# Kernel optimization log

Hardware: AMD Instinct MI355X
Metric: run time of the kernel (lower is better)

Reference implementation:

```python
import jax, jax.numpy as jnp
import numpy as np


def _bilinear_sample(plane, coords):
    """Bilinear grid_sample, align_corners=True, padding_mode='border'.
    plane: [C, S, S]; coords: [N, 2] with (x=width, y=height) in [-1, 1].
    Returns [N, C]."""
    C, S, _ = plane.shape
    scale = 0.5 * (S - 1)
    # align_corners=True mapping: -1 -> 0, +1 -> S-1; border padding == clamp
    px = jnp.clip((coords[:, 0] + 1.0) * scale, 0.0, S - 1.0)
    py = jnp.clip((coords[:, 1] + 1.0) * scale, 0.0, S - 1.0)
    x0 = jnp.floor(px).astype(jnp.int32)
    y0 = jnp.floor(py).astype(jnp.int32)
    x1 = jnp.minimum(x0 + 1, S - 1)
    y1 = jnp.minimum(y0 + 1, S - 1)
    wx = px - x0.astype(px.dtype)
    wy = py - y0.astype(py.dtype)
    v00 = plane[:, y0, x0]  # [C, N]
    v01 = plane[:, y0, x1]
    v10 = plane[:, y1, x0]
    v11 = plane[:, y1, x1]
    top = v00 * (1.0 - wx) + v01 * wx
    bot = v10 * (1.0 - wx) + v11 * wx
    return (top * (1.0 - wy) + bot * wy).T  # [N, C]


def setup_inputs() -> dict:
    key = jax.random.key(0)
    k1, k2 = jax.random.split(key)
    N, INDIM = 1000000, 4
    FDIM, FSIZE = 16, 1024
    P = INDIM * (INDIM - 1) // 2  # 6 plane pairs
    x = jax.random.uniform(k1, (N, INDIM), dtype=jnp.float32, minval=-1.0, maxval=1.0)
    fm = jax.random.normal(k2, (P, FDIM, FSIZE + 1, FSIZE + 1), dtype=jnp.float32) * 0.01
    return {"x": x, "fm": fm}


def reference(x, fm):
    N, indim = x.shape
    pairs = [(i, j) for i in range(indim - 1) for j in range(i + 1, indim)]
    ii = jnp.array([p[0] for p in pairs])
    jj = jnp.array([p[1] for p in pairs])
    # coords per plane pair: grid_sample convention (x=dim i, y=dim j)
    coords = jnp.stack([x[:, ii], x[:, jj]], axis=-1)      # [N, P, 2]
    coords = jnp.transpose(coords, (1, 0, 2))              # [P, N, 2]
    samples = jax.vmap(_bilinear_sample)(fm, coords)       # [P, N, fdim]
    # torch code concatenates pair features along dim 1 in pair order
    return jnp.transpose(samples, (1, 0, 2)).reshape(N, -1)  # [N, P*fdim]
```

## Files before the change

### kernel.cpp

```cpp
#include <hip/hip_runtime.h>
#include <stdint.h>


#define FP_S 1025
#define FP_C 16
#define FP_P 6

typedef float f32x4 __attribute__((ext_vector_type(4)));

__global__ __launch_bounds__(256) void fp_rowquant_v(const float* __restrict__ fm,
                                                     uint4* __restrict__ q8,
                                                     float* __restrict__ rs) {
    const size_t plane = (size_t)FP_S * FP_S;
    int y = blockIdx.x;
    int p = blockIdx.z;
    int t = threadIdx.x;
    const float* rowbase = fm + (size_t)p * FP_C * plane + (size_t)y * FP_S;

    f32x4 v[FP_C];
    float m = 0.0f;
#pragma unroll
    for (int c = 0; c < FP_C; ++c) {
        v[c] = *(const f32x4*)(rowbase + (size_t)c * plane + 4 * t);
        m = fmaxf(m, fmaxf(fmaxf(fabsf(v[c][0]), fabsf(v[c][1])),
                           fmaxf(fabsf(v[c][2]), fabsf(v[c][3]))));
    }
    float tail[FP_C];
    if (t == 255) {
#pragma unroll
        for (int c = 0; c < FP_C; ++c) {
            tail[c] = rowbase[(size_t)c * plane + 1024];
            m = fmaxf(m, fabsf(tail[c]));
        }
    }

    __shared__ float red[256];
    red[t] = m;
    __syncthreads();
#pragma unroll
    for (int s = 128; s > 0; s >>= 1) {
        if (t < s) red[t] = fmaxf(red[t], red[t + s]);
        __syncthreads();
    }
    float am = red[0];
    float inv = (am > 0.0f) ? 127.0f / am : 0.0f;
    if (t == 0) rs[p * FP_S + y] = am * (1.0f / 127.0f);

    uint4* qrow = q8 + (size_t)p * plane + (size_t)y * FP_S;
#pragma unroll
    for (int k = 0; k < 4; ++k) {
        uint32_t w[4];
#pragma unroll
        for (int r = 0; r < 4; ++r) {
            uint32_t acc = 0;
#pragma unroll
            for (int b = 0; b < 4; ++b) {
                int q = (int)rintf(v[4 * r + b][k] * inv);
                q = q > 127 ? 127 : (q < -127 ? -127 : q);
                acc |= ((uint32_t)(q & 0xff)) << (8 * b);
            }
            w[r] = acc;
        }
        qrow[4 * t + k] = make_uint4(w[0], w[1], w[2], w[3]);
    }
    if (t == 255) {
        uint32_t w[4];
#pragma unroll
        for (int r = 0; r < 4; ++r) {
            uint32_t acc = 0;
#pragma unroll
            for (int b = 0; b < 4; ++b) {
                int q = (int)rintf(tail[4 * r + b] * inv);
                q = q > 127 ? 127 : (q < -127 ? -127 : q);
                acc |= ((uint32_t)(q & 0xff)) << (8 * b);
            }
            w[r] = acc;
        }
        qrow[1024] = make_uint4(w[0], w[1], w[2], w[3]);
    }
}

__device__ __forceinline__ float fp_b8(uint32_t w, int b) {
    return (float)((int)(w << (24 - 8 * b)) >> 24);
}

__device__ __forceinline__ void fp_pair(int p, int& ii, int& jj) {
    switch (p) {
        case 0: ii = 0; jj = 1; break;
        case 1: ii = 0; jj = 2; break;
        case 2: ii = 0; jj = 3; break;
        case 3: ii = 1; jj = 2; break;
        case 4: ii = 1; jj = 3; break;
        default: ii = 2; jj = 3; break;
    }
}

__global__ __launch_bounds__(256) void fp_sample_q8r(const float* __restrict__ xin,
                                                     const uint4* __restrict__ q8,
                                                     const float* __restrict__ rs,
                                                     float* __restrict__ out, int N) {
    int n = blockIdx.x * 256 + threadIdx.x;
    if (n >= N) return;
    int p = blockIdx.z;
    int ii, jj;
    fp_pair(p, ii, jj);

    float4 xr = ((const float4*)xin)[n];
    float xv = (ii == 0) ? xr.x : ((ii == 1) ? xr.y : xr.z);
    float yv = (jj == 1) ? xr.y : ((jj == 2) ? xr.z : xr.w);

    float px = fminf(fmaxf((xv + 1.0f) * 512.0f, 0.0f), 1024.0f);
    float py = fminf(fmaxf((yv + 1.0f) * 512.0f, 0.0f), 1024.0f);
    float fx0 = floorf(px), fy0 = floorf(py);
    int x0 = (int)fx0, y0 = (int)fy0;
    int x1 = min(x0 + 1, FP_S - 1);
    int y1 = min(y0 + 1, FP_S - 1);
    float wx = px - fx0, wy = py - fy0;

    const float* prs = rs + p * FP_S;
    float s0 = prs[y0], s1 = prs[y1];
    float w00 = (1.0f - wx) * (1.0f - wy) * s0;
    float w01 = wx * (1.0f - wy) * s0;
    float w10 = (1.0f - wx) * wy * s1;
    float w11 = wx * wy * s1;

    const int plane = FP_S * FP_S;
    const uint4* pq = q8 + (size_t)p * plane;
    uint4 qa = pq[y0 * FP_S + x0];
    uint4 qb = pq[y0 * FP_S + x1];
    uint4 qc = pq[y1 * FP_S + x0];
    uint4 qd = pq[y1 * FP_S + x1];

    uint32_t wa[4] = {qa.x, qa.y, qa.z, qa.w};
    uint32_t wb[4] = {qb.x, qb.y, qb.z, qb.w};
    uint32_t wc[4] = {qc.x, qc.y, qc.z, qc.w};
    uint32_t wd[4] = {qd.x, qd.y, qd.z, qd.w};

    f32x4* o = (f32x4*)(out + (size_t)n * (FP_P * FP_C) + p * FP_C);
#pragma unroll
    for (int r = 0; r < 4; ++r) {
        f32x4 rr;
#pragma unroll
        for (int bb = 0; bb < 4; ++bb) {
            rr[bb] = w00 * fp_b8(wa[r], bb) + w01 * fp_b8(wb[r], bb) +
                     w10 * fp_b8(wc[r], bb) + w11 * fp_b8(wd[r], bb);
        }
        o[r] = rr;
    }
}

__global__ __launch_bounds__(256) void fp_sample_direct(const float* __restrict__ xin,
                                                        const float* __restrict__ fm,
                                                        float* __restrict__ out, int N) {
    int n = blockIdx.x * 256 + threadIdx.x;
    if (n >= N) return;
    int p = blockIdx.z;
    int ii, jj;
    fp_pair(p, ii, jj);

    float4 xr = ((const float4*)xin)[n];
    float xv = (ii == 0) ? xr.x : ((ii == 1) ? xr.y : xr.z);
    float yv = (jj == 1) ? xr.y : ((jj == 2) ? xr.z : xr.w);

    float px = fminf(fmaxf((xv + 1.0f) * 512.0f, 0.0f), 1024.0f);
    float py = fminf(fmaxf((yv + 1.0f) * 512.0f, 0.0f), 1024.0f);
    float fx0 = floorf(px), fy0 = floorf(py);
    int x0 = (int)fx0, y0 = (int)fy0;
    int x1 = min(x0 + 1, FP_S - 1);
    int y1 = min(y0 + 1, FP_S - 1);
    float wx = px - fx0, wy = py - fy0;
    float w00 = (1.0f - wx) * (1.0f - wy), w01 = wx * (1.0f - wy);
    float w10 = (1.0f - wx) * wy, w11 = wx * wy;

    const size_t plane = (size_t)FP_S * FP_S;
    const float* pl = fm + (size_t)p * FP_C * plane;
    float res[FP_C];
#pragma unroll
    for (int c = 0; c < FP_C; ++c) {
        const float* plc = pl + (size_t)c * plane;
        float a = plc[(size_t)y0 * FP_S + x0];
        float bq = plc[(size_t)y0 * FP_S + x1];
        float g = plc[(size_t)y1 * FP_S + x0];
        float d = plc[(size_t)y1 * FP_S + x1];
        res[c] = a * w00 + bq * w01 + g * w10 + d * w11;
    }
    f32x4* o = (f32x4*)(out + (size_t)n * (FP_P * FP_C) + p * FP_C);
#pragma unroll
    for (int k = 0; k < 4; ++k) {
        f32x4 r = {res[4 * k], res[4 * k + 1], res[4 * k + 2], res[4 * k + 3]};
        o[k] = r;
    }
}

static inline size_t fp_align(size_t v) { return (v + 255) & ~(size_t)255; }

extern "C" void kernel_launch(void* const* d_in, const int* in_sizes, int n_in,
                              void* d_out, int out_size, void* d_ws, size_t ws_size,
                              hipStream_t stream) {
    const float* x = (const float*)d_in[0];
    const float* fm = (const float*)d_in[1];
    float* out = (float*)d_out;
    int N = in_sizes[0] / 4;

    const size_t plane = (size_t)FP_S * FP_S;
    size_t q8_bytes = (size_t)FP_P * plane * 16;
    size_t rs_off = fp_align(q8_bytes);
    size_t needed = rs_off + (size_t)FP_P * FP_S * sizeof(float);

    if (ws_size >= needed) {
        uint4* q8 = (uint4*)d_ws;
        float* rs = (float*)((char*)d_ws + rs_off);

        dim3 gQ(FP_S, 1, FP_P);
        fp_rowquant_v<<<gQ, 256, 0, stream>>>(fm, q8, rs);

        dim3 gS((unsigned)((N + 255) / 256), 1, FP_P);
        fp_sample_q8r<<<gS, 256, 0, stream>>>(x, q8, rs, out, N);
    } else {
        dim3 gS((unsigned)((N + 255) / 256), 1, FP_P);
        fp_sample_direct<<<gS, 256, 0, stream>>>(x, fm, out, N);
    }
}
```

Measured before the change: 436.6 us.

## Quantize feature planes in 2x2 quad-tiled int8 layout with per-row-pair scales

Switches the int8 quantized plane from row-major texel order to a 2x2 quad-blocked layout, so the four bilinear neighbors of a sample usually fall in one contiguous 64-byte block. The per-row scale becomes a scale shared by each pair of rows, and the quantization kernel now handles two rows per 512-thread block. This aims to cut scattered cache-line traffic in the sampling kernel. In exchange, scales are coarser, which adds quantization error, and the padded last quad column adds a little workspace.

```diff
diff --git a/kernel.cpp b/kernel.cpp
--- a/kernel.cpp
+++ b/kernel.cpp
@@ -5,78 +5,100 @@
 #define FP_S 1025
 #define FP_C 16
 #define FP_P 6
-
+#define FP_Q 513
+
+typedef float f32x2 __attribute__((ext_vector_type(2)));
 typedef float f32x4 __attribute__((ext_vector_type(4)));
 
-__global__ __launch_bounds__(256) void fp_rowquant_v(const float* __restrict__ fm,
-                                                     uint4* __restrict__ q8,
-                                                     float* __restrict__ rs) {
+__device__ __forceinline__ int fp_qsat(float v, float inv) {
+    int q = (int)rintf(v * inv);
+    return q > 127 ? 127 : (q < -127 ? -127 : q);
+}
+
+__device__ __forceinline__ uint32_t fp_q4(float a, float b, float c, float d, float inv) {
+    return ((uint32_t)(fp_qsat(a, inv) & 0xff)) | ((uint32_t)(fp_qsat(b, inv) & 0xff) << 8) |
+           ((uint32_t)(fp_qsat(c, inv) & 0xff) << 16) | ((uint32_t)(fp_qsat(d, inv) & 0xff) << 24);
+}
+
+__device__ __forceinline__ uint4 fp_pack16v(const f32x2* v, int comp, float inv) {
+    uint4 r;
+    r.x = fp_q4(v[0][comp], v[1][comp], v[2][comp], v[3][comp], inv);
+    r.y = fp_q4(v[4][comp], v[5][comp], v[6][comp], v[7][comp], inv);
+    r.z = fp_q4(v[8][comp], v[9][comp], v[10][comp], v[11][comp], inv);
+    r.w = fp_q4(v[12][comp], v[13][comp], v[14][comp], v[15][comp], inv);
+    return r;
+}
+
+__device__ __forceinline__ uint4 fp_pack16s(const float* v, float inv) {
+    uint4 r;
+    r.x = fp_q4(v[0], v[1], v[2], v[3], inv);
+    r.y = fp_q4(v[4], v[5], v[6], v[7], inv);
+    r.z = fp_q4(v[8], v[9], v[10], v[11], inv);
+    r.w = fp_q4(v[12], v[13], v[14], v[15], inv);
+    return r;
+}
+
+__global__ __launch_bounds__(512) void fp_quadquant(const float* __restrict__ fm,
+                                                    uint4* __restrict__ q8,
+                                                    float* __restrict__ rs) {
     const size_t plane = (size_t)FP_S * FP_S;
-    int y = blockIdx.x;
+    int Y = blockIdx.x;
     int p = blockIdx.z;
     int t = threadIdx.x;
-    const float* rowbase = fm + (size_t)p * FP_C * plane + (size_t)y * FP_S;
-
-    f32x4 v[FP_C];
+    int y0 = 2 * Y;
+    bool hasy1 = (y0 + 1) < FP_S;
+    const float* pb = fm + (size_t)p * FP_C * plane;
+    const float* r0 = pb + (size_t)y0 * FP_S;
+    const float* r1 = hasy1 ? r0 + FP_S : r0;
+
+    f32x2 v0[FP_C], v1[FP_C];
     float m = 0.0f;
+    int x = 2 * t;
 #pragma unroll
     for (int c = 0; c < FP_C; ++c) {
-        v[c] = *(const f32x4*)(rowbase + (size_t)c * plane + 4 * t);
-        m = fmaxf(m, fmaxf(fmaxf(fabsf(v[c][0]), fabsf(v[c][1])),
-                           fmaxf(fabsf(v[c][2]), fabsf(v[c][3]))));
-    }
-    float tail[FP_C];
-    if (t == 255) {
+        v0[c] = *(const f32x2*)(r0 + (size_t)c * plane + x);
+        v1[c] = *(const f32x2*)(r1 + (size_t)c * plane + x);
+        m = fmaxf(m, fmaxf(fmaxf(fabsf(v0[c][0]), fabsf(v0[c][1])),
+                           fmaxf(fabsf(v1[c][0]), fabsf(v1[c][1]))));
+    }
+    if (t == 0) {
 #pragma unroll
         for (int c = 0; c < FP_C; ++c) {
-            tail[c] = rowbase[(size_t)c * plane + 1024];
-            m = fmaxf(m, fabsf(tail[c]));
+            m = fmaxf(m, fabsf(r0[(size_t)c * plane + 1024]));
+            m = fmaxf(m, fabsf(r1[(size_t)c * plane + 1024]));
         }
     }
 
-    __shared__ float red[256];
+    __shared__ float red[512];
     red[t] = m;
     __syncthreads();
 #pragma unroll
-    for (int s = 128; s > 0; s >>= 1) {
+    for (int s = 256; s > 0; s >>= 1) {
         if (t < s) red[t] = fmaxf(red[t], red[t + s]);
         __syncthreads();
     }
     float am = red[0];
     float inv = (am > 0.0f) ? 127.0f / am : 0.0f;
-    if (t == 0) rs[p * FP_S + y] = am * (1.0f / 127.0f);
-
-    uint4* qrow = q8 + (size_t)p * plane + (size_t)y * FP_S;
-#pragma unroll
-    for (int k = 0; k < 4; ++k) {
-        uint32_t w[4];
-#pragma unroll
-        for (int r = 0; r < 4; ++r) {
-            uint32_t acc = 0;
-#pragma unroll
-            for (int b = 0; b < 4; ++b) {
-                int q = (int)rintf(v[4 * r + b][k] * inv);
-                q = q > 127 ? 127 : (q < -127 ? -127 : q);
-                acc |= ((uint32_t)(q & 0xff)) << (8 * b);
-            }
-            w[r] = acc;
+    if (t == 0) rs[p * FP_Q + Y] = am * (1.0f / 127.0f);
+
+    uint4* qb_ = q8 + (((size_t)p * FP_Q + Y) * FP_Q + t) * 4;
+    qb_[0] = fp_pack16v(v0, 0, inv);
+    qb_[1] = fp_pack16v(v0, 1, inv);
+    qb_[2] = fp_pack16v(v1, 0, inv);
+    qb_[3] = fp_pack16v(v1, 1, inv);
+
+    if (t == 0) {
+        float c0[FP_C], c1[FP_C];
+#pragma unroll
+        for (int c = 0; c < FP_C; ++c) {
+            c0[c] = r0[(size_t)c * plane + 1024];
+            c1[c] = r1[(size_t)c * plane + 1024];
         }
-        qrow[4 * t + k] = make_uint4(w[0], w[1], w[2], w[3]);
-    }
-    if (t == 255) {
-        uint32_t w[4];
-#pragma unroll
-        for (int r = 0; r < 4; ++r) {
-            uint32_t acc = 0;
-#pragma unroll
-            for (int b = 0; b < 4; ++b) {
-                int q = (int)rintf(tail[4 * r + b] * inv);
-                q = q > 127 ? 127 : (q < -127 ? -127 : q);
-                acc |= ((uint32_t)(q & 0xff)) << (8 * b);
-            }
-            w[r] = acc;
-        }
-        qrow[1024] = make_uint4(w[0], w[1], w[2], w[3]);
+        uint4* qt = q8 + (((size_t)p * FP_Q + Y) * FP_Q + 512) * 4;
+        qt[0] = fp_pack16s(c0, inv);
+        qt[1] = make_uint4(0, 0, 0, 0);
+        qt[2] = fp_pack16s(c1, inv);
+        qt[3] = make_uint4(0, 0, 0, 0);
     }
 }
 
@@ -95,10 +117,10 @@
     }
 }
 
-__global__ __launch_bounds__(256) void fp_sample_q8r(const float* __restrict__ xin,
-                                                     const uint4* __restrict__ q8,
-                                                     const float* __restrict__ rs,
-                                                     float* __restrict__ out, int N) {
+__global__ __launch_bounds__(256) void fp_sample_qq(const float* __restrict__ xin,
+                                                    const uint4* __restrict__ q8,
+                                                    const float* __restrict__ rs,
+                                                    float* __restrict__ out, int N) {
     int n = blockIdx.x * 256 + threadIdx.x;
     if (n >= N) return;
     int p = blockIdx.z;
@@ -117,19 +139,22 @@
     int y1 = min(y0 + 1, FP_S - 1);
     float wx = px - fx0, wy = py - fy0;
 
-    const float* prs = rs + p * FP_S;
-    float s0 = prs[y0], s1 = prs[y1];
+    const float* prs = rs + p * FP_Q;
+    float s0 = prs[y0 >> 1], s1 = prs[y1 >> 1];
     float w00 = (1.0f - wx) * (1.0f - wy) * s0;
     float w01 = wx * (1.0f - wy) * s0;
     float w10 = (1.0f - wx) * wy * s1;
     float w11 = wx * wy * s1;
 
-    const int plane = FP_S * FP_S;
-    const uint4* pq = q8 + (size_t)p * plane;
-    uint4 qa = pq[y0 * FP_S + x0];
-    uint4 qb = pq[y0 * FP_S + x1];
-    uint4 qc = pq[y1 * FP_S + x0];
-    uint4 qd = pq[y1 * FP_S + x1];
+    const uint4* pq = q8 + (size_t)p * FP_Q * FP_Q * 4;
+    size_t ia = ((size_t)((y0 >> 1) * FP_Q + (x0 >> 1))) * 4 + ((y0 & 1) * 2 + (x0 & 1));
+    size_t ib = ((size_t)((y0 >> 1) * FP_Q + (x1 >> 1))) * 4 + ((y0 & 1) * 2 + (x1 & 1));
+    size_t ic = ((size_t)((y1 >> 1) * FP_Q + (x0 >> 1))) * 4 + ((y1 & 1) * 2 + (x0 & 1));
+    size_t id = ((size_t)((y1 >> 1) * FP_Q + (x1 >> 1))) * 4 + ((y1 & 1) * 2 + (x1 & 1));
+    uint4 qa = pq[ia];
+    uint4 qb = pq[ib];
+    uint4 qc = pq[ic];
+    uint4 qd = pq[id];
 
     uint32_t wa[4] = {qa.x, qa.y, qa.z, qa.w};
     uint32_t wb[4] = {qb.x, qb.y, qb.z, qb.w};
@@ -202,20 +227,19 @@
     float* out = (float*)d_out;
     int N = in_sizes[0] / 4;
 
-    const size_t plane = (size_t)FP_S * FP_S;
-    size_t q8_bytes = (size_t)FP_P * plane * 16;
+    size_t q8_bytes = (size_t)FP_P * FP_Q * FP_Q * 64;
     size_t rs_off = fp_align(q8_bytes);
-    size_t needed = rs_off + (size_t)FP_P * FP_S * sizeof(float);
+    size_t needed = rs_off + (size_t)FP_P * FP_Q * sizeof(float);
 
     if (ws_size >= needed) {
         uint4* q8 = (uint4*)d_ws;
         float* rs = (float*)((char*)d_ws + rs_off);
 
-        dim3 gQ(FP_S, 1, FP_P);
-        fp_rowquant_v<<<gQ, 256, 0, stream>>>(fm, q8, rs);
+        dim3 gQ(FP_Q, 1, FP_P);
+        fp_quadquant<<<gQ, 512, 0, stream>>>(fm, q8, rs);
 
         dim3 gS((unsigned)((N + 255) / 256), 1, FP_P);
-        fp_sample_q8r<<<gS, 256, 0, stream>>>(x, q8, rs, out, N);
+        fp_sample_qq<<<gS, 256, 0, stream>>>(x, q8, rs, out, N);
     } else {
         dim3 gS((unsigned)((N + 255) / 256), 1, FP_P);
         fp_sample_direct<<<gS, 256, 0, stream>>>(x, fm, out, N);
```

Result: no change. 429.5 us (-1.6%).
